# Performance work log

Hardware: AMD Instinct MI355X
Metric: run time of the kernel (lower is better)

Reference implementation:

```python
import jax, jax.numpy as jnp
import numpy as np

DIM = 256
RES = 64
SPLIT = 8
HEADS = 8
H_SP, W_SP = RES, SPLIT  # idx = 0 -> horizontal strips
HD = DIM // HEADS
SCALE = HD ** (-0.5)
WIN = H_SP * W_SP  # 512 tokens per window


def _to_windows(x, B, H, W, C):
    x = x.reshape(B, H // H_SP, H_SP, W // W_SP, W_SP, C)
    x = x.transpose(0, 1, 3, 2, 4, 5).reshape(-1, WIN, HEADS, HD)
    return x.transpose(0, 2, 1, 3)


def setup_inputs() -> dict:
    key = jax.random.key(0)
    k1, k2, k3 = jax.random.split(key, 3)
    qkv = jax.random.normal(k1, (3, 4, RES * RES, DIM), dtype=jnp.float32)
    conv_w = jax.random.normal(k2, (DIM, 1, 3, 3), dtype=jnp.float32) * 0.1
    conv_b = jax.random.normal(k3, (DIM,), dtype=jnp.float32) * 0.01
    return {"qkv": qkv, "conv_w": conv_w, "conv_b": conv_b}


def reference(qkv, conv_w, conv_b):
    q, k, v = qkv[0], qkv[1], qkv[2]
    B, L, C = q.shape
    H = W = RES
    qw = _to_windows(q, B, H, W, C) * SCALE
    kw = _to_windows(k, B, H, W, C)
    # v as per-window images [nWB, C, H_SP, W_SP] for depthwise LePE conv
    vimg = v.reshape(B, H // H_SP, H_SP, W // W_SP, W_SP, C)
    vimg = vimg.transpose(0, 1, 3, 5, 2, 4).reshape(-1, C, H_SP, W_SP)
    lepe = jax.lax.conv_general_dilated(
        vimg, conv_w, window_strides=(1, 1), padding='SAME',
        feature_group_count=C,
        dimension_numbers=('NCHW', 'OIHW', 'NCHW')) + conv_b[None, :, None, None]
    vw = vimg.reshape(-1, HEADS, HD, WIN).transpose(0, 1, 3, 2)
    lepe = lepe.reshape(-1, HEADS, HD, WIN).transpose(0, 1, 3, 2)
    attn = jax.nn.softmax(jnp.einsum('whqd,whkd->whqk', qw, kw), axis=-1)
    x = jnp.einsum('whqk,whkd->whqd', attn, vw) + lepe
    # windows -> image -> tokens (matches windows2img)
    x = x.transpose(0, 2, 1, 3).reshape(-1, WIN, C)
    x = x.reshape(B, H // H_SP, W // W_SP, H_SP, W_SP, C)
    x = x.transpose(0, 1, 3, 2, 4, 5).reshape(B, H * W, C)
    return x, attn
```

## Files before the change

kernel.cpp:

```cpp
#include <hip/hip_runtime.h>
#include <hip/hip_bf16.h>

typedef __attribute__((ext_vector_type(8))) __bf16 bf16x8;
typedef __attribute__((ext_vector_type(4))) float f32x4;


__global__ __launch_bounds__(256, 1)
void lepe_attn(const float* __restrict__ qkv,
               const float* __restrict__ conv_w,
               const float* __restrict__ conv_b,
               float* __restrict__ out)
{
    constexpr int kL = 4096, kC = 256, kHD = 32;
    constexpr int KSTR = 40;
    constexpr int VSTR = 520;
    constexpr int PSTR = 520;

    __shared__ __align__(16) __bf16 sK [512 * KSTR];
    __shared__ __align__(16) __bf16 sVt[ 32 * VSTR];
    __shared__ __align__(16) __bf16 sP [4 * 16 * PSTR];

    const int bx = blockIdx.x;
    const int wb = bx >> 3;
    const int h  = bx & 7;
    const int b  = wb >> 3;
    const int w  = wb & 7;
    const int tid  = threadIdx.x;
    const int lane = tid & 63;
    const int wave = tid >> 6;
    const int l15  = lane & 15;
    const int quad = lane >> 4;

    const float* kBase = qkv + (size_t)4 * kL * kC;
    const float* vBase = qkv + (size_t)8 * kL * kC;

    #pragma unroll
    for (int chunk = 0; chunk < 8; ++chunk) {
        int e  = chunk * 2048 + tid * 8;
        int t  = e >> 5;
        int d0 = e & 31;
        int l  = ((t >> 3) << 6) + (w << 3) + (t & 7);
        size_t g = ((size_t)(b * kL + l)) * kC + h * kHD + d0;
        f32x4 k0 = *(const f32x4*)(kBase + g);
        f32x4 k1 = *(const f32x4*)(kBase + g + 4);
        bf16x8 kk;
        kk[0] = (__bf16)k0[0]; kk[1] = (__bf16)k0[1];
        kk[2] = (__bf16)k0[2]; kk[3] = (__bf16)k0[3];
        kk[4] = (__bf16)k1[0]; kk[5] = (__bf16)k1[1];
        kk[6] = (__bf16)k1[2]; kk[7] = (__bf16)k1[3];
        *(bf16x8*)&sK[t * KSTR + d0] = kk;
        f32x4 v0 = *(const f32x4*)(vBase + g);
        f32x4 v1 = *(const f32x4*)(vBase + g + 4);
        sVt[(d0 + 0) * VSTR + t] = (__bf16)v0[0];
        sVt[(d0 + 1) * VSTR + t] = (__bf16)v0[1];
        sVt[(d0 + 2) * VSTR + t] = (__bf16)v0[2];
        sVt[(d0 + 3) * VSTR + t] = (__bf16)v0[3];
        sVt[(d0 + 4) * VSTR + t] = (__bf16)v1[0];
        sVt[(d0 + 5) * VSTR + t] = (__bf16)v1[1];
        sVt[(d0 + 6) * VSTR + t] = (__bf16)v1[2];
        sVt[(d0 + 7) * VSTR + t] = (__bf16)v1[3];
    }

    float w9[2][9], wbias[2];
    #pragma unroll
    for (int nt = 0; nt < 2; ++nt) {
        int c = h * kHD + nt * 16 + l15;
        #pragma unroll
        for (int k = 0; k < 9; ++k) w9[nt][k] = conv_w[c * 9 + k];
        wbias[nt] = conv_b[c];
    }

    __syncthreads();

    float* attnOut = out + (size_t)4 * kL * kC;
    __bf16* sPw = &sP[wave * 16 * PSTR];

    for (int qt = 0; qt < 8; ++qt) {
        const int qrow0 = qt * 64 + wave * 16;

        int tq = qrow0 + l15;
        int lq = ((tq >> 3) << 6) + (w << 3) + (tq & 7);
        const float* qp = qkv + ((size_t)(b * kL + lq)) * kC + h * kHD + quad * 8;
        f32x4 q0 = *(const f32x4*)qp;
        f32x4 q1 = *(const f32x4*)(qp + 4);
        bf16x8 a_frag;
        a_frag[0] = (__bf16)q0[0]; a_frag[1] = (__bf16)q0[1];
        a_frag[2] = (__bf16)q0[2]; a_frag[3] = (__bf16)q0[3];
        a_frag[4] = (__bf16)q1[0]; a_frag[5] = (__bf16)q1[1];
        a_frag[6] = (__bf16)q1[2]; a_frag[7] = (__bf16)q1[3];

        f32x4 accS[32];
        const f32x4 zf = {0.f, 0.f, 0.f, 0.f};
        #pragma unroll
        for (int nt = 0; nt < 32; ++nt) {
            bf16x8 b_frag = *(const bf16x8*)&sK[(nt * 16 + l15) * KSTR + quad * 8];
            accS[nt] = __builtin_amdgcn_mfma_f32_16x16x32_bf16(a_frag, b_frag, zf, 0, 0, 0);
        }

        float mr[4] = {-3.0e38f, -3.0e38f, -3.0e38f, -3.0e38f};
        #pragma unroll
        for (int nt = 0; nt < 32; ++nt) {
            #pragma unroll
            for (int r = 0; r < 4; ++r) {
                float sv = accS[nt][r] * 0.17677669529663687f;
                accS[nt][r] = sv;
                mr[r] = fmaxf(mr[r], sv);
            }
        }
        #pragma unroll
        for (int r = 0; r < 4; ++r) {
            mr[r] = fmaxf(mr[r], __shfl_xor(mr[r], 1));
            mr[r] = fmaxf(mr[r], __shfl_xor(mr[r], 2));
            mr[r] = fmaxf(mr[r], __shfl_xor(mr[r], 4));
            mr[r] = fmaxf(mr[r], __shfl_xor(mr[r], 8));
        }
        float sr[4] = {0.f, 0.f, 0.f, 0.f};
        #pragma unroll
        for (int nt = 0; nt < 32; ++nt) {
            #pragma unroll
            for (int r = 0; r < 4; ++r) {
                float e = __expf(accS[nt][r] - mr[r]);
                accS[nt][r] = e;
                sr[r] += e;
            }
        }
        float inv[4];
        #pragma unroll
        for (int r = 0; r < 4; ++r) {
            sr[r] += __shfl_xor(sr[r], 1);
            sr[r] += __shfl_xor(sr[r], 2);
            sr[r] += __shfl_xor(sr[r], 4);
            sr[r] += __shfl_xor(sr[r], 8);
            inv[r] = 1.0f / sr[r];
        }

        const size_t attnRowBase = (size_t)bx * 512 * 512 + (size_t)(qrow0 + quad * 4) * 512;
        #pragma unroll
        for (int nt = 0; nt < 32; ++nt) {
            int col = nt * 16 + l15;
            #pragma unroll
            for (int r = 0; r < 4; ++r) {
                float p = accS[nt][r] * inv[r];
                attnOut[attnRowBase + (size_t)r * 512 + col] = p;
                sPw[(quad * 4 + r) * PSTR + col] = (__bf16)p;
            }
        }

        f32x4 accO0 = {0.f, 0.f, 0.f, 0.f}, accO1 = {0.f, 0.f, 0.f, 0.f};
        #pragma unroll
        for (int kt = 0; kt < 16; ++kt) {
            bf16x8 pa  = *(const bf16x8*)&sPw[l15 * PSTR + kt * 32 + quad * 8];
            bf16x8 vb0 = *(const bf16x8*)&sVt[ l15        * VSTR + kt * 32 + quad * 8];
            bf16x8 vb1 = *(const bf16x8*)&sVt[(16 + l15) * VSTR + kt * 32 + quad * 8];
            accO0 = __builtin_amdgcn_mfma_f32_16x16x32_bf16(pa, vb0, accO0, 0, 0, 0);
            accO1 = __builtin_amdgcn_mfma_f32_16x16x32_bf16(pa, vb1, accO1, 0, 0, 0);
        }

        const int t0  = qrow0 + quad * 4;
        const int r0  = t0 >> 3;
        const int cw0 = t0 & 7;
        #pragma unroll
        for (int nt = 0; nt < 2; ++nt) {
            const int dch = nt * 16 + l15;
            float patch[3][6];
            #pragma unroll
            for (int i = 0; i < 3; ++i) {
                int r2 = r0 - 1 + i;
                #pragma unroll
                for (int j = 0; j < 6; ++j) {
                    int c2 = cw0 - 1 + j;
                    bool ok = (r2 >= 0) && (r2 < 64) && (c2 >= 0) && (c2 < 8);
                    patch[i][j] = ok ? (float)sVt[dch * VSTR + r2 * 8 + c2] : 0.0f;
                }
            }
            #pragma unroll
            for (int r = 0; r < 4; ++r) {
                float acc = (nt ? accO1[r] : accO0[r]) + wbias[nt];
                #pragma unroll
                for (int i = 0; i < 3; ++i)
                    #pragma unroll
                    for (int jj = 0; jj < 3; ++jj)
                        acc += w9[nt][i * 3 + jj] * patch[i][r + jj];
                int trow = t0 + r;
                int lo = ((trow >> 3) << 6) + (w << 3) + (trow & 7);
                out[((size_t)(b * kL + lo)) * kC + h * kHD + dch] = acc;
            }
        }
    }
}

extern "C" void kernel_launch(void* const* d_in, const int* in_sizes, int n_in,
                              void* d_out, int out_size, void* d_ws, size_t ws_size,
                              hipStream_t stream) {
    const float* qkv = (const float*)d_in[0];
    const float* cw  = (const float*)d_in[1];
    const float* cb  = (const float*)d_in[2];
    float* outp = (float*)d_out;
    lepe_attn<<<dim3(256), dim3(256), 0, stream>>>(qkv, cw, cb, outp);
}
```

Before: 337.7 us.

## Transpose score MFMA, stage probabilities through LDS, and double waves per block

The block now runs 512 threads, so each wave handles four 16-row query tiles. Swapping the MFMA operands lets each lane own a whole query column, which makes the softmax reductions cheaper. The scale is folded into Q before the bf16 conversion, and the V transpose load is vectorised into whole bf16x8 LDS rows. Probabilities go into LDS as bf16 in two halves and are read back for vectorised f32x4 stores of the attention matrix. The risk is precision: the stored attention weights are now bf16-rounded rather than full fp32.

```diff
diff --git a/kernel.cpp b/kernel.cpp
--- a/kernel.cpp
+++ b/kernel.cpp
@@ -2,27 +2,29 @@
 #include <hip/hip_bf16.h>
 
 typedef __attribute__((ext_vector_type(8))) __bf16 bf16x8;
+typedef __attribute__((ext_vector_type(4))) __bf16 bf16x4;
 typedef __attribute__((ext_vector_type(4))) float f32x4;
 
 
-__global__ __launch_bounds__(256, 1)
+__global__ __launch_bounds__(512, 2)
 void lepe_attn(const float* __restrict__ qkv,
                const float* __restrict__ conv_w,
                const float* __restrict__ conv_b,
                float* __restrict__ out)
 {
-    constexpr int kL = 4096, kC = 256, kHD = 32;
+    constexpr int kL = 4096, kC = 256;
     constexpr int KSTR = 40;
     constexpr int VSTR = 520;
-    constexpr int PSTR = 520;
+    constexpr int PSTR = 264;
+    constexpr float SCALE = 0.17677669529663687f;
 
     __shared__ __align__(16) __bf16 sK [512 * KSTR];
     __shared__ __align__(16) __bf16 sVt[ 32 * VSTR];
-    __shared__ __align__(16) __bf16 sP [4 * 16 * PSTR];
+    __shared__ __align__(16) __bf16 sP [8 * 16 * PSTR];
 
     const int bx = blockIdx.x;
+    const int h  = bx & 7;
     const int wb = bx >> 3;
-    const int h  = bx & 7;
     const int b  = wb >> 3;
     const int w  = wb & 7;
     const int tid  = threadIdx.x;
@@ -34,37 +36,43 @@
     const float* kBase = qkv + (size_t)4 * kL * kC;
     const float* vBase = qkv + (size_t)8 * kL * kC;
 
-    #pragma unroll
-    for (int chunk = 0; chunk < 8; ++chunk) {
-        int e  = chunk * 2048 + tid * 8;
-        int t  = e >> 5;
-        int d0 = e & 31;
-        int l  = ((t >> 3) << 6) + (w << 3) + (t & 7);
-        size_t g = ((size_t)(b * kL + l)) * kC + h * kHD + d0;
-        f32x4 k0 = *(const f32x4*)(kBase + g);
-        f32x4 k1 = *(const f32x4*)(kBase + g + 4);
-        bf16x8 kk;
-        kk[0] = (__bf16)k0[0]; kk[1] = (__bf16)k0[1];
-        kk[2] = (__bf16)k0[2]; kk[3] = (__bf16)k0[3];
-        kk[4] = (__bf16)k1[0]; kk[5] = (__bf16)k1[1];
-        kk[6] = (__bf16)k1[2]; kk[7] = (__bf16)k1[3];
-        *(bf16x8*)&sK[t * KSTR + d0] = kk;
-        f32x4 v0 = *(const f32x4*)(vBase + g);
-        f32x4 v1 = *(const f32x4*)(vBase + g + 4);
-        sVt[(d0 + 0) * VSTR + t] = (__bf16)v0[0];
-        sVt[(d0 + 1) * VSTR + t] = (__bf16)v0[1];
-        sVt[(d0 + 2) * VSTR + t] = (__bf16)v0[2];
-        sVt[(d0 + 3) * VSTR + t] = (__bf16)v0[3];
-        sVt[(d0 + 4) * VSTR + t] = (__bf16)v1[0];
-        sVt[(d0 + 5) * VSTR + t] = (__bf16)v1[1];
-        sVt[(d0 + 6) * VSTR + t] = (__bf16)v1[2];
-        sVt[(d0 + 7) * VSTR + t] = (__bf16)v1[3];
+    {
+        const int d0 = (tid & 3) * 8;
+        const int t0 = (tid >> 2) * 4;
+        #pragma unroll
+        for (int i = 0; i < 4; ++i) {
+            int t = t0 + i;
+            int l = ((t >> 3) << 6) + (w << 3) + (t & 7);
+            const float* p = kBase + ((size_t)(b * kL + l)) * kC + h * 32 + d0;
+            f32x4 x0 = *(const f32x4*)p;
+            f32x4 x1 = *(const f32x4*)(p + 4);
+            bf16x8 kk;
+            kk[0]=(__bf16)x0[0]; kk[1]=(__bf16)x0[1]; kk[2]=(__bf16)x0[2]; kk[3]=(__bf16)x0[3];
+            kk[4]=(__bf16)x1[0]; kk[5]=(__bf16)x1[1]; kk[6]=(__bf16)x1[2]; kk[7]=(__bf16)x1[3];
+            *(bf16x8*)&sK[t * KSTR + d0] = kk;
+        }
+    }
+    {
+        const int d0 = (tid & 7) * 4;
+        const int t0 = (tid >> 3) * 8;
+        const int lrow = ((t0 >> 3) << 6) + (w << 3);
+        const float* p = vBase + ((size_t)(b * kL + lrow)) * kC + h * 32 + d0;
+        f32x4 vv[8];
+        #pragma unroll
+        for (int i = 0; i < 8; ++i) vv[i] = *(const f32x4*)(p + (size_t)i * kC);
+        #pragma unroll
+        for (int j = 0; j < 4; ++j) {
+            bf16x8 row;
+            #pragma unroll
+            for (int i = 0; i < 8; ++i) row[i] = (__bf16)vv[i][j];
+            *(bf16x8*)&sVt[(d0 + j) * VSTR + t0] = row;
+        }
     }
 
     float w9[2][9], wbias[2];
     #pragma unroll
     for (int nt = 0; nt < 2; ++nt) {
-        int c = h * kHD + nt * 16 + l15;
+        int c = h * 32 + nt * 16 + l15;
         #pragma unroll
         for (int k = 0; k < 9; ++k) w9[nt][k] = conv_w[c * 9 + k];
         wbias[nt] = conv_b[c];
@@ -75,85 +83,78 @@
     float* attnOut = out + (size_t)4 * kL * kC;
     __bf16* sPw = &sP[wave * 16 * PSTR];
 
-    for (int qt = 0; qt < 8; ++qt) {
-        const int qrow0 = qt * 64 + wave * 16;
+    for (int qt = 0; qt < 4; ++qt) {
+        const int qrow0 = (wave * 4 + qt) * 16;
 
         int tq = qrow0 + l15;
         int lq = ((tq >> 3) << 6) + (w << 3) + (tq & 7);
-        const float* qp = qkv + ((size_t)(b * kL + lq)) * kC + h * kHD + quad * 8;
+        const float* qp = qkv + ((size_t)(b * kL + lq)) * kC + h * 32 + quad * 8;
         f32x4 q0 = *(const f32x4*)qp;
         f32x4 q1 = *(const f32x4*)(qp + 4);
-        bf16x8 a_frag;
-        a_frag[0] = (__bf16)q0[0]; a_frag[1] = (__bf16)q0[1];
-        a_frag[2] = (__bf16)q0[2]; a_frag[3] = (__bf16)q0[3];
-        a_frag[4] = (__bf16)q1[0]; a_frag[5] = (__bf16)q1[1];
-        a_frag[6] = (__bf16)q1[2]; a_frag[7] = (__bf16)q1[3];
+        bf16x8 qfrag;
+        qfrag[0]=(__bf16)(q0[0]*SCALE); qfrag[1]=(__bf16)(q0[1]*SCALE);
+        qfrag[2]=(__bf16)(q0[2]*SCALE); qfrag[3]=(__bf16)(q0[3]*SCALE);
+        qfrag[4]=(__bf16)(q1[0]*SCALE); qfrag[5]=(__bf16)(q1[1]*SCALE);
+        qfrag[6]=(__bf16)(q1[2]*SCALE); qfrag[7]=(__bf16)(q1[3]*SCALE);
 
         f32x4 accS[32];
         const f32x4 zf = {0.f, 0.f, 0.f, 0.f};
         #pragma unroll
         for (int nt = 0; nt < 32; ++nt) {
-            bf16x8 b_frag = *(const bf16x8*)&sK[(nt * 16 + l15) * KSTR + quad * 8];
-            accS[nt] = __builtin_amdgcn_mfma_f32_16x16x32_bf16(a_frag, b_frag, zf, 0, 0, 0);
-        }
-
-        float mr[4] = {-3.0e38f, -3.0e38f, -3.0e38f, -3.0e38f};
-        #pragma unroll
-        for (int nt = 0; nt < 32; ++nt) {
+            bf16x8 kfrag = *(const bf16x8*)&sK[(nt * 16 + l15) * KSTR + quad * 8];
+            accS[nt] = __builtin_amdgcn_mfma_f32_16x16x32_bf16(kfrag, qfrag, zf, 0, 0, 0);
+        }
+
+        float m = -3.0e38f;
+        #pragma unroll
+        for (int nt = 0; nt < 32; ++nt)
+            #pragma unroll
+            for (int r = 0; r < 4; ++r) m = fmaxf(m, accS[nt][r]);
+        m = fmaxf(m, __shfl_xor(m, 16));
+        m = fmaxf(m, __shfl_xor(m, 32));
+        float s = 0.f;
+        #pragma unroll
+        for (int nt = 0; nt < 32; ++nt)
             #pragma unroll
             for (int r = 0; r < 4; ++r) {
-                float sv = accS[nt][r] * 0.17677669529663687f;
-                accS[nt][r] = sv;
-                mr[r] = fmaxf(mr[r], sv);
-            }
-        }
-        #pragma unroll
-        for (int r = 0; r < 4; ++r) {
-            mr[r] = fmaxf(mr[r], __shfl_xor(mr[r], 1));
-            mr[r] = fmaxf(mr[r], __shfl_xor(mr[r], 2));
-            mr[r] = fmaxf(mr[r], __shfl_xor(mr[r], 4));
-            mr[r] = fmaxf(mr[r], __shfl_xor(mr[r], 8));
-        }
-        float sr[4] = {0.f, 0.f, 0.f, 0.f};
-        #pragma unroll
-        for (int nt = 0; nt < 32; ++nt) {
-            #pragma unroll
-            for (int r = 0; r < 4; ++r) {
-                float e = __expf(accS[nt][r] - mr[r]);
+                float e = __expf(accS[nt][r] - m);
                 accS[nt][r] = e;
-                sr[r] += e;
-            }
-        }
-        float inv[4];
-        #pragma unroll
-        for (int r = 0; r < 4; ++r) {
-            sr[r] += __shfl_xor(sr[r], 1);
-            sr[r] += __shfl_xor(sr[r], 2);
-            sr[r] += __shfl_xor(sr[r], 4);
-            sr[r] += __shfl_xor(sr[r], 8);
-            inv[r] = 1.0f / sr[r];
-        }
-
-        const size_t attnRowBase = (size_t)bx * 512 * 512 + (size_t)(qrow0 + quad * 4) * 512;
-        #pragma unroll
-        for (int nt = 0; nt < 32; ++nt) {
-            int col = nt * 16 + l15;
-            #pragma unroll
-            for (int r = 0; r < 4; ++r) {
-                float p = accS[nt][r] * inv[r];
-                attnOut[attnRowBase + (size_t)r * 512 + col] = p;
-                sPw[(quad * 4 + r) * PSTR + col] = (__bf16)p;
-            }
-        }
-
-        f32x4 accO0 = {0.f, 0.f, 0.f, 0.f}, accO1 = {0.f, 0.f, 0.f, 0.f};
-        #pragma unroll
-        for (int kt = 0; kt < 16; ++kt) {
-            bf16x8 pa  = *(const bf16x8*)&sPw[l15 * PSTR + kt * 32 + quad * 8];
-            bf16x8 vb0 = *(const bf16x8*)&sVt[ l15        * VSTR + kt * 32 + quad * 8];
-            bf16x8 vb1 = *(const bf16x8*)&sVt[(16 + l15) * VSTR + kt * 32 + quad * 8];
-            accO0 = __builtin_amdgcn_mfma_f32_16x16x32_bf16(pa, vb0, accO0, 0, 0, 0);
-            accO1 = __builtin_amdgcn_mfma_f32_16x16x32_bf16(pa, vb1, accO1, 0, 0, 0);
+                s += e;
+            }
+        s += __shfl_xor(s, 16);
+        s += __shfl_xor(s, 32);
+        const float inv = 1.0f / s;
+
+        f32x4 accO0 = {0.f,0.f,0.f,0.f}, accO1 = {0.f,0.f,0.f,0.f};
+        #pragma unroll
+        for (int p = 0; p < 2; ++p) {
+            #pragma unroll
+            for (int ntl = 0; ntl < 16; ++ntl) {
+                const f32x4 a = accS[p * 16 + ntl];
+                bf16x4 pk;
+                pk[0]=(__bf16)(a[0]*inv); pk[1]=(__bf16)(a[1]*inv);
+                pk[2]=(__bf16)(a[2]*inv); pk[3]=(__bf16)(a[3]*inv);
+                *(bf16x4*)&sPw[l15 * PSTR + ntl * 16 + quad * 4] = pk;
+            }
+            #pragma unroll
+            for (int ktl = 0; ktl < 8; ++ktl) {
+                bf16x8 pa  = *(const bf16x8*)&sPw[l15 * PSTR + ktl * 32 + quad * 8];
+                const int c0 = p * 256 + ktl * 32 + quad * 8;
+                bf16x8 vb0 = *(const bf16x8*)&sVt[ l15        * VSTR + c0];
+                bf16x8 vb1 = *(const bf16x8*)&sVt[(16 + l15) * VSTR + c0];
+                accO0 = __builtin_amdgcn_mfma_f32_16x16x32_bf16(pa, vb0, accO0, 0, 0, 0);
+                accO1 = __builtin_amdgcn_mfma_f32_16x16x32_bf16(pa, vb1, accO1, 0, 0, 0);
+            }
+            const int row = lane >> 2;
+            const int cof = (lane & 3) * 4;
+            const size_t rbase = ((size_t)bx * 512 + qrow0 + row) * 512 + p * 256 + cof;
+            #pragma unroll
+            for (int u = 0; u < 16; ++u) {
+                bf16x4 pv = *(const bf16x4*)&sPw[row * PSTR + u * 16 + cof];
+                f32x4 o;
+                o[0]=(float)pv[0]; o[1]=(float)pv[1]; o[2]=(float)pv[2]; o[3]=(float)pv[3];
+                *(f32x4*)&attnOut[rbase + u * 16] = o;
+            }
         }
 
         const int t0  = qrow0 + quad * 4;
@@ -183,7 +184,7 @@
                         acc += w9[nt][i * 3 + jj] * patch[i][r + jj];
                 int trow = t0 + r;
                 int lo = ((trow >> 3) << 6) + (w << 3) + (trow & 7);
-                out[((size_t)(b * kL + lo)) * kC + h * kHD + dch] = acc;
+                out[((size_t)(b * kL + lo)) * kC + h * 32 + dch] = acc;
             }
         }
     }
@@ -196,5 +197,5 @@
     const float* cw  = (const float*)d_in[1];
     const float* cb  = (const float*)d_in[2];
     float* outp = (float*)d_out;
-    lepe_attn<<<dim3(256), dim3(256), 0, stream>>>(qkv, cw, cb, outp);
+    lepe_attn<<<dim3(256), dim3(512), 0, stream>>>(qkv, cw, cb, outp);
 }
```

Result: slower. 388.7 us (+15.1%).
